# Optimization experiments

Hardware: AMD Instinct MI355X
Metric: run time of the kernel (lower is better)

Reference implementation:

```python
import jax, jax.numpy as jnp
import numpy as np


def setup_inputs() -> dict:
    key = jax.random.key(0)
    k1, k2 = jax.random.split(key)
    N, D, G = 1000000, 128, 4096
    x = jax.random.normal(k1, (N, D), dtype=jnp.float32)
    batch = jnp.sort(jax.random.randint(k2, (N,), 0, G, dtype=jnp.int64))
    return {"x": x, "batch": batch, "num_graphs": G}


def reference(x, batch, num_graphs):
    # Single-pass segment max: [num_nodes, D] -> [num_graphs, D]
    # (equivalent to torch per-graph masked max, but O(N) scatter-reduce)
    return jax.ops.segment_max(x, batch, num_segments=num_graphs)
```

## Files before the change

kernel.cpp:

```cpp
#include <hip/hip_runtime.h>

typedef float float4v __attribute__((ext_vector_type(4)));

#define DIM 128

__global__ __launch_bounds__(256, 8) void segmax_block_kernel(
    const float* __restrict__ x, const int* __restrict__ batch,
    float* __restrict__ out, int N)
{
    __shared__ float red[4][DIM];

    int seg = blockIdx.x;
    int tid = threadIdx.x;
    int w = tid >> 6;
    int lane = tid & 63;
    int half = lane >> 5;
    int c = (lane & 31) * 4;

    int g = seg + (lane & 1);
    int lo = 0, hi = N;
    while (lo < hi) {
        int mid = (lo + hi) >> 1;
        if (batch[mid] < g) lo = mid + 1; else hi = mid;
    }
    int r0 = __shfl(lo, 0);
    int r1 = __shfl(lo, 1);

    float4v acc;
    acc.x = -INFINITY; acc.y = -INFINITY; acc.z = -INFINITY; acc.w = -INFINITY;

    const float* xc = x + c;
    int r = r0 + 2 * w + half;

    for (; r + 24 < r1; r += 32) {
        float4v v0 = *(const float4v*)(xc + (size_t)r * DIM);
        float4v v1 = *(const float4v*)(xc + (size_t)(r + 8) * DIM);
        float4v v2 = *(const float4v*)(xc + (size_t)(r + 16) * DIM);
        float4v v3 = *(const float4v*)(xc + (size_t)(r + 24) * DIM);
        acc.x = fmaxf(fmaxf(acc.x, v0.x), fmaxf(v1.x, v2.x));
        acc.y = fmaxf(fmaxf(acc.y, v0.y), fmaxf(v1.y, v2.y));
        acc.z = fmaxf(fmaxf(acc.z, v0.z), fmaxf(v1.z, v2.z));
        acc.w = fmaxf(fmaxf(acc.w, v0.w), fmaxf(v1.w, v2.w));
        acc.x = fmaxf(acc.x, v3.x);
        acc.y = fmaxf(acc.y, v3.y);
        acc.z = fmaxf(acc.z, v3.z);
        acc.w = fmaxf(acc.w, v3.w);
    }
    for (; r < r1; r += 8) {
        float4v v = *(const float4v*)(xc + (size_t)r * DIM);
        acc.x = fmaxf(acc.x, v.x);
        acc.y = fmaxf(acc.y, v.y);
        acc.z = fmaxf(acc.z, v.z);
        acc.w = fmaxf(acc.w, v.w);
    }

    acc.x = fmaxf(acc.x, __shfl_xor(acc.x, 32));
    acc.y = fmaxf(acc.y, __shfl_xor(acc.y, 32));
    acc.z = fmaxf(acc.z, __shfl_xor(acc.z, 32));
    acc.w = fmaxf(acc.w, __shfl_xor(acc.w, 32));

    if (half == 0) {
        *(float4v*)&red[w][c] = acc;
    }
    __syncthreads();
    if (tid < 32) {
        int cc = tid * 4;
        float4v a = *(const float4v*)&red[0][cc];
        float4v b = *(const float4v*)&red[1][cc];
        float4v d = *(const float4v*)&red[2][cc];
        float4v e = *(const float4v*)&red[3][cc];
        a.x = fmaxf(fmaxf(a.x, b.x), fmaxf(d.x, e.x));
        a.y = fmaxf(fmaxf(a.y, b.y), fmaxf(d.y, e.y));
        a.z = fmaxf(fmaxf(a.z, b.z), fmaxf(d.z, e.z));
        a.w = fmaxf(fmaxf(a.w, b.w), fmaxf(d.w, e.w));
        *(float4v*)(out + (size_t)seg * DIM + cc) = a;
    }
}

extern "C" void kernel_launch(void* const* d_in, const int* in_sizes, int n_in,
                              void* d_out, int out_size, void* d_ws, size_t ws_size,
                              hipStream_t stream) {
    const float* x = (const float*)d_in[0];
    const int* batch = (const int*)d_in[1];
    float* out = (float*)d_out;

    int N = in_sizes[1];
    int G = out_size / DIM;

    segmax_block_kernel<<<G, 256, 0, stream>>>(x, batch, out, N);
}
```

Measured before the change: 102.9 us.

## Replace serial binary search with wave-cooperative ballot search and halve block size

Segment boundary lookup now uses a 32-way parallel search per half-wave with ballot/popcount over four rounds instead of a per-lane serial binary search, cutting dependent global load latency at kernel start. Blocks shrink from 256 to 128 threads with row strides adjusted accordingly, so each thread processes twice as many rows. This trades intra-block parallelism for lower launch/search overhead and more resident blocks.

New measurement: 99.25 us. 1.04x faster.

```diff
diff --git a/kernel.cpp b/kernel.cpp
--- a/kernel.cpp
+++ b/kernel.cpp
@@ -4,39 +4,59 @@
 
 #define DIM 128
 
-__global__ __launch_bounds__(256, 8) void segmax_block_kernel(
+__global__ __launch_bounds__(128, 8) void segmax_kernel(
     const float* __restrict__ x, const int* __restrict__ batch,
     float* __restrict__ out, int N)
 {
-    __shared__ float red[4][DIM];
+    __shared__ float red[2][DIM];
 
-    int seg = blockIdx.x;
-    int tid = threadIdx.x;
-    int w = tid >> 6;
+    int seg  = blockIdx.x;
+    int tid  = threadIdx.x;
+    int w    = tid >> 6;
     int lane = tid & 63;
-    int half = lane >> 5;
-    int c = (lane & 31) * 4;
+    int sub  = lane & 31;
+    int which = lane >> 5;
+    int c    = sub * 4;
 
-    int g = seg + (lane & 1);
-    int lo = 0, hi = N;
-    while (lo < hi) {
-        int mid = (lo + hi) >> 1;
-        if (batch[mid] < g) lo = mid + 1; else hi = mid;
+    int g = seg + which;
+    unsigned long long gmask = which ? 0xFFFFFFFF00000000ULL : 0x00000000FFFFFFFFULL;
+    int lo = 0, len = N;
+    #pragma unroll
+    for (int it = 0; it < 4; ++it) {
+        int L = len;
+        int p = lo + ((sub * L) >> 5);
+        int pos = min(p, N - 1);
+        bool pred = (L > 0) && (batch[pos] < g);
+        unsigned long long bal = __ballot(pred);
+        int cnt = __popcll(bal & gmask);
+        if (L > 32) {
+            int nlo = (cnt == 0)  ? lo       : (lo + (((cnt - 1) * L) >> 5) + 1);
+            int pc  = (cnt == 32) ? (lo + L) : (lo + ((cnt * L) >> 5));
+            lo = nlo;
+            len = pc - nlo;
+        }
+    }
+    {
+        int pos = min(lo + ((sub < len) ? sub : 0), N - 1);
+        bool pred = (sub < len) && (batch[pos] < g);
+        unsigned long long bal = __ballot(pred);
+        lo += __popcll(bal & gmask);
     }
     int r0 = __shfl(lo, 0);
-    int r1 = __shfl(lo, 1);
+    int r1 = __shfl(lo, 32);
 
     float4v acc;
     acc.x = -INFINITY; acc.y = -INFINITY; acc.z = -INFINITY; acc.w = -INFINITY;
 
     const float* xc = x + c;
+    int half = which;
     int r = r0 + 2 * w + half;
 
-    for (; r + 24 < r1; r += 32) {
+    for (; r + 12 < r1; r += 16) {
         float4v v0 = *(const float4v*)(xc + (size_t)r * DIM);
-        float4v v1 = *(const float4v*)(xc + (size_t)(r + 8) * DIM);
-        float4v v2 = *(const float4v*)(xc + (size_t)(r + 16) * DIM);
-        float4v v3 = *(const float4v*)(xc + (size_t)(r + 24) * DIM);
+        float4v v1 = *(const float4v*)(xc + (size_t)(r + 4) * DIM);
+        float4v v2 = *(const float4v*)(xc + (size_t)(r + 8) * DIM);
+        float4v v3 = *(const float4v*)(xc + (size_t)(r + 12) * DIM);
         acc.x = fmaxf(fmaxf(acc.x, v0.x), fmaxf(v1.x, v2.x));
         acc.y = fmaxf(fmaxf(acc.y, v0.y), fmaxf(v1.y, v2.y));
         acc.z = fmaxf(fmaxf(acc.z, v0.z), fmaxf(v1.z, v2.z));
@@ -46,7 +66,7 @@
         acc.z = fmaxf(acc.z, v3.z);
         acc.w = fmaxf(acc.w, v3.w);
     }
-    for (; r < r1; r += 8) {
+    for (; r < r1; r += 4) {
         float4v v = *(const float4v*)(xc + (size_t)r * DIM);
         acc.x = fmaxf(acc.x, v.x);
         acc.y = fmaxf(acc.y, v.y);
@@ -67,12 +87,10 @@
         int cc = tid * 4;
         float4v a = *(const float4v*)&red[0][cc];
         float4v b = *(const float4v*)&red[1][cc];
-        float4v d = *(const float4v*)&red[2][cc];
-        float4v e = *(const float4v*)&red[3][cc];
-        a.x = fmaxf(fmaxf(a.x, b.x), fmaxf(d.x, e.x));
-        a.y = fmaxf(fmaxf(a.y, b.y), fmaxf(d.y, e.y));
-        a.z = fmaxf(fmaxf(a.z, b.z), fmaxf(d.z, e.z));
-        a.w = fmaxf(fmaxf(a.w, b.w), fmaxf(d.w, e.w));
+        a.x = fmaxf(a.x, b.x);
+        a.y = fmaxf(a.y, b.y);
+        a.z = fmaxf(a.z, b.z);
+        a.w = fmaxf(a.w, b.w);
         *(float4v*)(out + (size_t)seg * DIM + cc) = a;
     }
 }
@@ -87,5 +105,5 @@
     int N = in_sizes[1];
     int G = out_size / DIM;
 
-    segmax_block_kernel<<<G, 256, 0, stream>>>(x, batch, out, N);
+    segmax_kernel<<<G, 128, 0, stream>>>(x, batch, out, N);
 }
```
